# Kernel tuning notes

Hardware: AMD Instinct MI355X
Metric: run time of the kernel (lower is better)

The kernel has to match this reference:

```python
import jax, jax.numpy as jnp
import numpy as np

B, L, D, H, FF = 8, 512, 1024, 16, 4096
HD = D // H
EPS = 1e-5

def ste_round(x):
    # straight-through rounding (QAT)
    return x + jax.lax.stop_gradient(jnp.round(x) - x)

def fq_act(x):
    # 8-bit asymmetric per-tensor fake quant with dynamic min/max observer
    lo = jnp.minimum(jnp.min(x), 0.0)
    hi = jnp.maximum(jnp.max(x), 0.0)
    scale = jax.lax.stop_gradient(jnp.maximum((hi - lo) / 255.0, 1e-8))
    zp = jax.lax.stop_gradient(jnp.round(-lo / scale))
    q = jnp.clip(ste_round(x / scale) + zp, 0.0, 255.0)
    return (q - zp) * scale

def fq_w(w):
    # 8-bit symmetric per-tensor fake quant for weights
    scale = jax.lax.stop_gradient(jnp.maximum(jnp.max(jnp.abs(w)) / 127.0, 1e-8))
    q = jnp.clip(ste_round(w / scale), -128.0, 127.0)
    return q * scale

def qlinear(x, w, b):
    # QuantizedLayer: fake-quant weight, linear, fake-quant output activation
    return fq_act(jnp.einsum('...i,oi->...o', x, fq_w(w)) + b)

def layer_norm(x, g, b):
    mu = jnp.mean(x, axis=-1, keepdims=True)
    var = jnp.mean(jnp.square(x - mu), axis=-1, keepdims=True)
    return (x - mu) * jax.lax.rsqrt(var + EPS) * g + b

def setup_inputs() -> dict:
    key = jax.random.key(0)
    ks = jax.random.split(key, 8)
    s = 0.02
    return {
        'x': jax.random.normal(ks[0], (B, L, D), jnp.float32),
        'ln1_g': jnp.ones((D,), jnp.float32), 'ln1_b': jnp.zeros((D,), jnp.float32),
        'wq': jax.random.normal(ks[1], (D, D), jnp.float32) * s, 'bq': jnp.zeros((D,), jnp.float32),
        'wk': jax.random.normal(ks[2], (D, D), jnp.float32) * s, 'bk': jnp.zeros((D,), jnp.float32),
        'wv': jax.random.normal(ks[3], (D, D), jnp.float32) * s, 'bv': jnp.zeros((D,), jnp.float32),
        'wo': jax.random.normal(ks[4], (D, D), jnp.float32) * s, 'bo': jnp.zeros((D,), jnp.float32),
        'ln2_g': jnp.ones((D,), jnp.float32), 'ln2_b': jnp.zeros((D,), jnp.float32),
        'w_fc': jax.random.normal(ks[5], (FF, D), jnp.float32) * s, 'b_fc': jnp.zeros((FF,), jnp.float32),
        'w_proj': jax.random.normal(ks[6], (D, FF), jnp.float32) * s, 'b_proj': jnp.zeros((D,), jnp.float32),
    }

def reference(x, ln1_g, ln1_b, wq, bq, wk, bk, wv, bv, wo, bo,
              ln2_g, ln2_b, w_fc, b_fc, w_proj, b_proj):
    # --- attention sub-block ---
    h = layer_norm(x, ln1_g, ln1_b)
    def heads(t):  # [B,L,D] -> [B,H,L,HD]
        return t.reshape(B, L, H, HD).transpose(0, 2, 1, 3)
    # QuantizedLayer output fq + post_act fake quant (applied twice, per source)
    q = fq_act(heads(qlinear(h, wq, bq)))
    k = fq_act(heads(qlinear(h, wk, bk)))
    v = fq_act(heads(qlinear(h, wv, bv)))
    scale = 1.0 / np.sqrt(HD).astype(np.float32)
    attn = jnp.einsum('bhld,bhmd->bhlm', q, k) * scale  # [B,H,L,L]
    attn = jax.nn.softmax(attn, axis=-1)
    attn = fq_act(attn)  # softmax post-act fake quant (dropout p=0 is identity)
    ctx = jnp.einsum('bhlm,bhmd->bhld', attn, v)
    ctx = ctx.transpose(0, 2, 1, 3).reshape(B, L, D)
    x = x + qlinear(ctx, wo, bo)
    # --- MLP sub-block ---
    h2 = layer_norm(x, ln2_g, ln2_b)
    h2 = qlinear(h2, w_fc, b_fc)
    h2 = jax.nn.gelu(h2, approximate=False)  # torch nn.GELU default (erf)
    x = x + qlinear(h2, w_proj, b_proj)
    return x
```

## Files before the change

### kernel.cpp

```cpp
#include <hip/hip_runtime.h>
#include <cmath>

#define BB 8
#define LL 512
#define DD 1024
#define HH 16
#define HDD 64
#define FFD 4096
#define MTOK (BB*LL)
#define EPSF 1e-5f
#define BK 64

typedef __attribute__((ext_vector_type(8))) short bf16x8;
typedef __attribute__((ext_vector_type(4))) float f32x4;


struct WSet {
  const float* w[6];
  unsigned short* q[6];
  int n4[6];
};

__device__ inline void atomicMaxPos(float* addr, float v) {
  atomicMax((unsigned int*)addr, __float_as_uint(v));
}

__device__ inline unsigned short f2bf(float x) {
  unsigned int u = __float_as_uint(x);
  u += 0x7fffu + ((u >> 16) & 1u);
  return (unsigned short)(u >> 16);
}
__device__ inline float bf2f(unsigned short h) {
  return __uint_as_float((unsigned int)h << 16);
}

__device__ __forceinline__ void gld16(const unsigned short* g, unsigned short* l) {
  __builtin_amdgcn_global_load_lds(
      (const __attribute__((address_space(1))) unsigned int*)g,
      (__attribute__((address_space(3))) unsigned int*)l, 16, 0, 0);
}

__global__ void k_init_bcat(float* __restrict__ s, const float* __restrict__ b0,
                            const float* __restrict__ b1, const float* __restrict__ b2,
                            float* __restrict__ dst) {
  int i = blockIdx.x * blockDim.x + threadIdx.x;
  if (i < 256) s[i] = 0.0f;
  if (i < 3072) dst[i] = i < 1024 ? b0[i] : (i < 2048 ? b1[i - 1024] : b2[i - 2048]);
}

__global__ void k_absmax6(WSet ws, float* __restrict__ scal) {
  const int id = blockIdx.y;
  const float4* w4 = (const float4*)ws.w[id];
  const int n4 = ws.n4[id];
  float m = 0.0f;
  for (int i = blockIdx.x * blockDim.x + threadIdx.x; i < n4; i += gridDim.x * blockDim.x) {
    float4 v = w4[i];
    m = fmaxf(m, fmaxf(fmaxf(fabsf(v.x), fabsf(v.y)), fmaxf(fabsf(v.z), fabsf(v.w))));
  }
  #pragma unroll
  for (int o = 32; o; o >>= 1) m = fmaxf(m, __shfl_down(m, o, 64));
  __shared__ float sb[4];
  int lane = threadIdx.x & 63, wid = threadIdx.x >> 6;
  if (lane == 0) sb[wid] = m;
  __syncthreads();
  if (threadIdx.x == 0) atomicMaxPos(scal + id, fmaxf(fmaxf(sb[0], sb[1]), fmaxf(sb[2], sb[3])));
}

__global__ void k_quantw6(WSet ws, const float* __restrict__ scal) {
  const int id = blockIdx.y;
  float s = fmaxf(scal[id] / 127.0f, 1e-8f);
  const float4* w4 = (const float4*)ws.w[id];
  ushort4* q4 = (ushort4*)ws.q[id];
  const int n4 = ws.n4[id];
  for (int i = blockIdx.x * blockDim.x + threadIdx.x; i < n4; i += gridDim.x * blockDim.x) {
    float4 v = w4[i];
    ushort4 o;
    o.x = f2bf(fminf(fmaxf(rintf(v.x / s), -128.0f), 127.0f));
    o.y = f2bf(fminf(fmaxf(rintf(v.y / s), -128.0f), 127.0f));
    o.z = f2bf(fminf(fmaxf(rintf(v.z / s), -128.0f), 127.0f));
    o.w = f2bf(fminf(fmaxf(rintf(v.w / s), -128.0f), 127.0f));
    q4[i] = o;
  }
}

__device__ inline float2 fq_params(const float* sHi, const float* sNeg) {
  float hi = *sHi, lo = -(*sNeg);
  float scale = fmaxf((hi - lo) / 255.0f, 1e-8f);
  float zp = rintf(-lo / scale);
  return make_float2(scale, zp);
}
__device__ inline float fq1(float x, float scale, float zp) {
  float q = fminf(fmaxf(rintf(x / scale) + zp, 0.0f), 255.0f);
  return (q - zp) * scale;
}
__device__ inline float2 fq_params2(const float* sHi, const float* sNeg) {
  float2 p1 = fq_params(sHi, sNeg);
  float hi2 = fq1(*sHi, p1.x, p1.y);
  float lo2 = fq1(-(*sNeg), p1.x, p1.y);
  float scale = fmaxf((hi2 - lo2) / 255.0f, 1e-8f);
  float zp = rintf(-lo2 / scale);
  return make_float2(scale, zp);
}
__device__ inline float code2(float x, float2 p1, float2 p2) {
  float v1 = fq1(x, p1.x, p1.y);
  float q = fminf(fmaxf(rintf(v1 / p2.x) + p2.y, 0.0f), 255.0f);
  return q - p2.y;
}

__global__ void k_quant_codes(const float* __restrict__ src, int colBase,
                              unsigned short* __restrict__ oc, const float* __restrict__ sl) {
  float2 p1 = fq_params(sl, sl + 1);
  float2 p2 = fq_params2(sl, sl + 1);
  const int n4 = MTOK * DD / 4;
  for (int i = blockIdx.x * blockDim.x + threadIdx.x; i < n4; i += gridDim.x * blockDim.x) {
    int row = i >> 8, c = (i & 255) * 4;
    float4 v = *(const float4*)(src + (size_t)row * 3072 + colBase + c);
    ushort4 o;
    o.x = f2bf(code2(v.x, p1, p2)); o.y = f2bf(code2(v.y, p1, p2));
    o.z = f2bf(code2(v.z, p1, p2)); o.w = f2bf(code2(v.w, p1, p2));
    *(ushort4*)&oc[(size_t)row * DD + c] = o;
  }
}

__global__ __launch_bounds__(256) void k_quant_codes_vt(
    const float* __restrict__ src, unsigned short* __restrict__ vt,
    const float* __restrict__ sl) {
  __shared__ unsigned short tile[64 * 68];
  float2 p1 = fq_params(sl, sl + 1);
  float2 p2 = fq_params2(sl, sl + 1);
  const int m0 = blockIdx.x * 64, h = blockIdx.y, b = blockIdx.z;
  const int t = threadIdx.x;
  const int r = t >> 2, c0 = (t & 3) * 16;
  const float* s4 = src + ((size_t)(b * LL + m0 + r)) * 3072 + 2048 + h * HDD + c0;
  #pragma unroll
  for (int i = 0; i < 4; ++i) {
    float4 v = *(const float4*)(s4 + i * 4);
    ushort4 o;
    o.x = f2bf(code2(v.x, p1, p2)); o.y = f2bf(code2(v.y, p1, p2));
    o.z = f2bf(code2(v.z, p1, p2)); o.w = f2bf(code2(v.w, p1, p2));
    *(ushort4*)&tile[r * 68 + c0 + i * 4] = o;
  }
  __syncthreads();
  const int dr = t >> 2, ms = (t & 3) * 16;
  unsigned short* dst = vt + ((size_t)((b * HH + h) * HDD + dr)) * LL + m0 + ms;
  #pragma unroll
  for (int i = 0; i < 4; ++i) {
    ushort4 o;
    o.x = tile[(ms + i * 4 + 0) * 68 + dr];
    o.y = tile[(ms + i * 4 + 1) * 68 + dr];
    o.z = tile[(ms + i * 4 + 2) * 68 + dr];
    o.w = tile[(ms + i * 4 + 3) * 68 + dr];
    *(ushort4*)(dst + i * 4) = o;
  }
}

__global__ void k_sum_minmax(const float* __restrict__ parts, size_t pstride4, int np,
                             const float* __restrict__ bias, int n4, int cmask,
                             float* __restrict__ sl) {
  float hi = 0.0f, ng = 0.0f;
  for (int i = blockIdx.x * blockDim.x + threadIdx.x; i < n4; i += gridDim.x * blockDim.x) {
    float4 bc = *(const float4*)(bias + (i & cmask) * 4);
    float vx = bc.x, vy = bc.y, vz = bc.z, vw = bc.w;
    for (int j = 0; j < np; ++j) {
      float4 a = ((const float4*)parts)[j * pstride4 + i];
      vx += a.x; vy += a.y; vz += a.z; vw += a.w;
    }
    hi = fmaxf(hi, fmaxf(fmaxf(vx, vy), fmaxf(vz, vw)));
    ng = fmaxf(ng, fmaxf(fmaxf(-vx, -vy), fmaxf(-vz, -vw)));
  }
  #pragma unroll
  for (int o = 32; o; o >>= 1) {
    hi = fmaxf(hi, __shfl_down(hi, o, 64));
    ng = fmaxf(ng, __shfl_down(ng, o, 64));
  }
  __shared__ float sh[4], sn[4];
  int lane = threadIdx.x & 63, wid = threadIdx.x >> 6;
  if (lane == 0) { sh[wid] = hi; sn[wid] = ng; }
  __syncthreads();
  if (threadIdx.x == 0) {
    atomicMaxPos(sl, fmaxf(fmaxf(sh[0], sh[1]), fmaxf(sh[2], sh[3])));
    atomicMaxPos(sl + 1, fmaxf(fmaxf(sn[0], sn[1]), fmaxf(sn[2], sn[3])));
  }
}

__global__ void k_quant_res2(const float* __restrict__ parts, size_t pstride4, int np,
                             const float* __restrict__ bias, const float* __restrict__ res,
                             float* __restrict__ out, int n4, int cmask,
                             const float* __restrict__ sl) {
  float2 p = fq_params(sl, sl + 1);
  for (int i = blockIdx.x * blockDim.x + threadIdx.x; i < n4; i += gridDim.x * blockDim.x) {
    float4 bc = *(const float4*)(bias + (i & cmask) * 4);
    float vx = bc.x, vy = bc.y, vz = bc.z, vw = bc.w;
    for (int j = 0; j < np; ++j) {
      float4 a = ((const float4*)parts)[j * pstride4 + i];
      vx += a.x; vy += a.y; vz += a.z; vw += a.w;
    }
    float4 r = ((const float4*)res)[i];
    float4 o;
    o.x = r.x + fq1(vx, p.x, p.y);
    o.y = r.y + fq1(vy, p.x, p.y);
    o.z = r.z + fq1(vz, p.x, p.y);
    o.w = r.w + fq1(vw, p.x, p.y);
    ((float4*)out)[i] = o;
  }
}

__device__ inline float gelu_exact(float g) {
  return 0.5f * g * (1.0f + erff(g * 0.7071067811865475f));
}

__global__ void k_gelu_codes(const float* __restrict__ x,
                             unsigned short* __restrict__ ghi, unsigned short* __restrict__ glo,
                             int n4, const float* __restrict__ sl) {
  float2 p = fq_params(sl, sl + 1);
  for (int i = blockIdx.x * blockDim.x + threadIdx.x; i < n4; i += gridDim.x * blockDim.x) {
    float4 v = ((const float4*)x)[i];
    float g0 = gelu_exact(fq1(v.x, p.x, p.y)), g1 = gelu_exact(fq1(v.y, p.x, p.y));
    float g2 = gelu_exact(fq1(v.z, p.x, p.y)), g3 = gelu_exact(fq1(v.w, p.x, p.y));
    ushort4 h, l;
    h.x = f2bf(g0); l.x = f2bf(g0 - bf2f(h.x));
    h.y = f2bf(g1); l.y = f2bf(g1 - bf2f(h.y));
    h.z = f2bf(g2); l.z = f2bf(g2 - bf2f(h.z));
    h.w = f2bf(g3); l.w = f2bf(g3 - bf2f(h.w));
    ((ushort4*)ghi)[i] = h;
    ((ushort4*)glo)[i] = l;
  }
}

__device__ inline float block_sum256(float v, float* sb) {
  #pragma unroll
  for (int o = 32; o; o >>= 1) v += __shfl_down(v, o, 64);
  int lane = threadIdx.x & 63, wid = threadIdx.x >> 6;
  __syncthreads();
  if (lane == 0) sb[wid] = v;
  __syncthreads();
  return sb[0] + sb[1] + sb[2] + sb[3];
}

__global__ __launch_bounds__(256) void k_ln_bf(const float* __restrict__ x, const float* __restrict__ g,
                                               const float* __restrict__ bta,
                                               unsigned short* __restrict__ ohi,
                                               unsigned short* __restrict__ olo) {
  __shared__ float sb[4];
  int row = blockIdx.x;
  const float4* xr = (const float4*)(x + (size_t)row * DD);
  float4 v = xr[threadIdx.x];
  float mu = block_sum256(v.x + v.y + v.z + v.w, sb) * (1.0f / DD);
  float dx = v.x - mu, dy = v.y - mu, dz = v.z - mu, dw = v.w - mu;
  float var = block_sum256(dx*dx + dy*dy + dz*dz + dw*dw, sb) * (1.0f / DD);
  float rs = 1.0f / sqrtf(var + EPSF);
  float4 gv = ((const float4*)g)[threadIdx.x];
  float4 bv = ((const float4*)bta)[threadIdx.x];
  float o0 = dx * rs * gv.x + bv.x;
  float o1 = dy * rs * gv.y + bv.y;
  float o2 = dz * rs * gv.z + bv.z;
  float o3 = dw * rs * gv.w + bv.w;
  ushort4 h, l;
  h.x = f2bf(o0); l.x = f2bf(o0 - bf2f(h.x));
  h.y = f2bf(o1); l.y = f2bf(o1 - bf2f(h.y));
  h.z = f2bf(o2); l.z = f2bf(o2 - bf2f(h.z));
  h.w = f2bf(o3); l.w = f2bf(o3 - bf2f(h.w));
  ((ushort4*)(ohi + (size_t)row * DD))[threadIdx.x] = h;
  ((ushort4*)(olo + (size_t)row * DD))[threadIdx.x] = l;
}

__global__ __launch_bounds__(256) void k_res_ln(
    const float* __restrict__ parts, size_t pstride4,
    const float* __restrict__ bias, const float* __restrict__ res,
    float* __restrict__ x1, const float* __restrict__ sl,
    const float* __restrict__ g, const float* __restrict__ bta,
    unsigned short* __restrict__ ohi, unsigned short* __restrict__ olo) {
  __shared__ float sb[4];
  float2 p = fq_params(sl, sl + 1);
  int row = blockIdx.x, t = threadIdx.x;
  size_t i4 = (size_t)row * 256 + t;
  float4 a = ((const float4*)parts)[i4];
  float4 b = ((const float4*)parts)[pstride4 + i4];
  float4 bc = ((const float4*)bias)[t];
  float4 r = ((const float4*)res)[i4];
  float4 xv;
  xv.x = r.x + fq1(a.x + b.x + bc.x, p.x, p.y);
  xv.y = r.y + fq1(a.y + b.y + bc.y, p.x, p.y);
  xv.z = r.z + fq1(a.z + b.z + bc.z, p.x, p.y);
  xv.w = r.w + fq1(a.w + b.w + bc.w, p.x, p.y);
  ((float4*)x1)[i4] = xv;
  float mu = block_sum256(xv.x + xv.y + xv.z + xv.w, sb) * (1.0f / DD);
  float dx = xv.x - mu, dy = xv.y - mu, dz = xv.z - mu, dw = xv.w - mu;
  float var = block_sum256(dx*dx + dy*dy + dz*dz + dw*dw, sb) * (1.0f / DD);
  float rs = 1.0f / sqrtf(var + EPSF);
  float4 gv = ((const float4*)g)[t];
  float4 bv = ((const float4*)bta)[t];
  float o0 = dx * rs * gv.x + bv.x;
  float o1 = dy * rs * gv.y + bv.y;
  float o2 = dz * rs * gv.z + bv.z;
  float o3 = dw * rs * gv.w + bv.w;
  ushort4 h, l;
  h.x = f2bf(o0); l.x = f2bf(o0 - bf2f(h.x));
  h.y = f2bf(o1); l.y = f2bf(o1 - bf2f(h.y));
  h.z = f2bf(o2); l.z = f2bf(o2 - bf2f(h.z));
  h.w = f2bf(o3); l.w = f2bf(o3 - bf2f(h.w));
  ((ushort4*)(ohi + (size_t)row * DD))[t] = h;
  ((ushort4*)(olo + (size_t)row * DD))[t] = l;
}

__global__ __launch_bounds__(256, 3) void k_gemm_bf(
    const unsigned short* __restrict__ Ahi, const unsigned short* __restrict__ Alo,
    const unsigned short* __restrict__ Bq,
    const float* __restrict__ bias, const float* __restrict__ wsc, float* __restrict__ obs,
    float* __restrict__ C, int ldC, int K, int kLen, int segShift, size_t partStride) {
  __shared__ unsigned short sAh[128 * BK];
  __shared__ unsigned short sAl[128 * BK];
  __shared__ unsigned short sB [128 * BK];
  __shared__ float redH, redN;
  const int t = threadIdx.x;
  const int row0 = blockIdx.x * 128, col0 = blockIdx.y * 128;
  const int kOff = blockIdx.z * kLen;
  float* Cp = C + (size_t)blockIdx.z * partStride;
  const int wave = t >> 6, lane = t & 63;
  const int wr = (wave >> 1) * 64, wc = (wave & 1) * 64;
  const int fr = lane & 15, fq = lane >> 4;
  const int seg = col0 >> segShift;
  const float s = fmaxf(wsc[seg] / 127.0f, 1e-8f);
  if (t == 0) { redH = 0.f; redN = 0.f; }

  f32x4 acc[4][4];
  #pragma unroll
  for (int i = 0; i < 4; ++i)
    #pragma unroll
    for (int j = 0; j < 4; ++j) acc[i][j] = (f32x4){0.f, 0.f, 0.f, 0.f};

  const int srB = lane >> 3;
  const int scs = lane & 7;

  for (int k0 = kOff; k0 < kOff + kLen; k0 += BK) {
    __syncthreads();
    #pragma unroll
    for (int it = 0; it < 4; ++it) {
      int r = (wave * 4 + it) * 8 + srB;
      int g = scs ^ (r & 7);
      size_t ga = (size_t)(row0 + r) * K + k0 + g * 8;
      size_t gb = (size_t)(col0 + r) * K + k0 + g * 8;
      int ld = r * BK + scs * 8;
      gld16(Ahi + ga, &sAh[ld]);
      gld16(Alo + ga, &sAl[ld]);
      gld16(Bq + gb, &sB[ld]);
    }
    __syncthreads();
    #pragma unroll
    for (int hh = 0; hh < 2; ++hh) {
      bf16x8 ah[4], al[4], bb[4];
      #pragma unroll
      for (int i = 0; i < 4; ++i) {
        int Ra = wr + i * 16 + fr;
        int Rb = wc + i * 16 + fr;
        int ca = ((hh * 4 + fq) ^ (Ra & 7)) * 8;
        int cb = ((hh * 4 + fq) ^ (Rb & 7)) * 8;
        ah[i] = *(const bf16x8*)&sAh[Ra * BK + ca];
        al[i] = *(const bf16x8*)&sAl[Ra * BK + ca];
        bb[i] = *(const bf16x8*)&sB [Rb * BK + cb];
      }
      #pragma unroll
      for (int i = 0; i < 4; ++i)
        #pragma unroll
        for (int j = 0; j < 4; ++j) {
          acc[i][j] = __builtin_amdgcn_mfma_f32_16x16x32_bf16(ah[i], bb[j], acc[i][j], 0, 0, 0);
          acc[i][j] = __builtin_amdgcn_mfma_f32_16x16x32_bf16(al[i], bb[j], acc[i][j], 0, 0, 0);
        }
    }
  }

  float ohi = 0.f, ong = 0.f;
  #pragma unroll
  for (int i = 0; i < 4; ++i) {
    #pragma unroll
    for (int j = 0; j < 4; ++j) {
      int col = col0 + wc + j * 16 + fr;
      float bcol = bias ? bias[col] : 0.0f;
      #pragma unroll
      for (int rg = 0; rg < 4; ++rg) {
        int row = row0 + wr + i * 16 + fq * 4 + rg;
        float val = acc[i][j][rg] * s + bcol;
        if (obs) { ohi = fmaxf(ohi, val); ong = fmaxf(ong, -val); }
        Cp[(size_t)row * ldC + col] = val;
      }
    }
  }
  if (obs) {
    #pragma unroll
    for (int o = 32; o; o >>= 1) {
      ohi = fmaxf(ohi, __shfl_down(ohi, o, 64));
      ong = fmaxf(ong, __shfl_down(ong, o, 64));
    }
    if (lane == 0) { atomicMaxPos(&redH, ohi); atomicMaxPos(&redN, ong); }
    __syncthreads();
    if (t == 0) {
      atomicMaxPos(obs + 2 * seg, redH);
      atomicMaxPos(obs + 2 * seg + 1, redN);
    }
  }
}

__global__ __launch_bounds__(256) void k_attn_a_mfma(
    const unsigned short* __restrict__ qc, const unsigned short* __restrict__ kc,
    const float* __restrict__ slq, const float* __restrict__ slk,
    float* __restrict__ rowm, float* __restrict__ rowz, float* __restrict__ maxp) {
  __shared__ unsigned short ks[64 * 72];
  __shared__ float redp;
  const int t = threadIdx.x, wave = t >> 6, lane = t & 63;
  const int fr = lane & 15, fq = lane >> 4;
  const int l0 = blockIdx.x * 64, h = blockIdx.y, b = blockIdx.z;
  const float sfac = fq_params2(slq, slq + 1).x * fq_params2(slk, slk + 1).x * 0.125f;
  if (t == 0) redp = 0.f;
  const unsigned short* qrow = qc + ((size_t)(b * LL + l0 + wave * 16 + fr)) * DD + h * HDD;
  bf16x8 qa0 = *(const bf16x8*)(qrow + fq * 8);
  bf16x8 qa1 = *(const bf16x8*)(qrow + 32 + fq * 8);
  float mrun[4] = {-INFINITY, -INFINITY, -INFINITY, -INFINITY};
  float zrun[4] = {0.f, 0.f, 0.f, 0.f};
  for (int mc = 0; mc < LL; mc += 64) {
    __syncthreads();
    #pragma unroll
    for (int it = 0; it < 2; ++it) {
      int si = t + it * 256, r = si >> 3, c8 = (si & 7) * 8;
      *(bf16x8*)&ks[r * 72 + c8] =
          *(const bf16x8*)(kc + ((size_t)(b * LL + mc + r)) * DD + h * HDD + c8);
    }
    __syncthreads();
    float sv[4][4];
    #pragma unroll
    for (int j = 0; j < 4; ++j) {
      bf16x8 b0 = *(const bf16x8*)&ks[(j * 16 + fr) * 72 + fq * 8];
      bf16x8 b1 = *(const bf16x8*)&ks[(j * 16 + fr) * 72 + 32 + fq * 8];
      f32x4 sAcc = (f32x4){0.f, 0.f, 0.f, 0.f};
      sAcc = __builtin_amdgcn_mfma_f32_16x16x32_bf16(qa0, b0, sAcc, 0, 0, 0);
      sAcc = __builtin_amdgcn_mfma_f32_16x16x32_bf16(qa1, b1, sAcc, 0, 0, 0);
      #pragma unroll
      for (int rg = 0; rg < 4; ++rg) sv[j][rg] = sAcc[rg] * sfac;
    }
    #pragma unroll
    for (int rg = 0; rg < 4; ++rg) {
      float nm = mrun[rg];
      #pragma unroll
      for (int j = 0; j < 4; ++j) nm = fmaxf(nm, sv[j][rg]);
      float z = zrun[rg] * expf(mrun[rg] - nm);
      #pragma unroll
      for (int j = 0; j < 4; ++j) z += expf(sv[j][rg] - nm);
      zrun[rg] = z; mrun[rg] = nm;
    }
  }
  #pragma unroll
  for (int off = 1; off < 16; off <<= 1) {
    #pragma unroll
    for (int rg = 0; rg < 4; ++rg) {
      float om = __shfl_xor(mrun[rg], off, 64);
      float oz = __shfl_xor(zrun[rg], off, 64);
      float nm = fmaxf(mrun[rg], om);
      zrun[rg] = zrun[rg] * expf(mrun[rg] - nm) + oz * expf(om - nm);
      mrun[rg] = nm;
    }
  }
  if (fr == 0) {
    int rid = (b * HH + h) * LL + l0 + wave * 16 + fq * 4;
    float lmax = 0.f;
    #pragma unroll
    for (int rg = 0; rg < 4; ++rg) {
      rowm[rid + rg] = mrun[rg]; rowz[rid + rg] = zrun[rg];
      lmax = fmaxf(lmax, 1.0f / zrun[rg]);
    }
    atomicMaxPos(&redp, lmax);
  }
  __syncthreads();
  if (t == 0) atomicMaxPos(maxp, redp);
}

__global__ __launch_bounds__(256) void k_attn_b_mfma(
    const unsigned short* __restrict__ qc, const unsigned short* __restrict__ kc,
    const unsigned short* __restrict__ vt,
    const float* __restrict__ slq, const float* __restrict__ slk, const float* __restrict__ slv,
    const float* __restrict__ rowm, const float* __restrict__ rowz,
    const float* __restrict__ maxp,
    unsigned short* __restrict__ chi, unsigned short* __restrict__ clo) {
  __shared__ unsigned short ks[64 * 72];
  __shared__ unsigned short vs[64 * 72];
  __shared__ unsigned short ps[4][16 * 72];
  const int t = threadIdx.x, wave = t >> 6, lane = t & 63;
  const int fr = lane & 15, fq = lane >> 4;
  const int l0 = blockIdx.x * 64, h = blockIdx.y, b = blockIdx.z;
  const float sfac = fq_params2(slq, slq + 1).x * fq_params2(slk, slk + 1).x * 0.125f;
  const float sv2 = fq_params2(slv, slv + 1).x;
  const float pscale = fmaxf(maxp[0] / 255.0f, 1e-8f);
  const float ipscale = 1.0f / pscale;
  const int ridb = (b * HH + h) * LL + l0 + wave * 16 + fq * 4;
  float rm[4], rzi[4];
  #pragma unroll
  for (int rg = 0; rg < 4; ++rg) { rm[rg] = rowm[ridb + rg]; rzi[rg] = 1.0f / rowz[ridb + rg]; }
  const unsigned short* qrow = qc + ((size_t)(b * LL + l0 + wave * 16 + fr)) * DD + h * HDD;
  bf16x8 qa0 = *(const bf16x8*)(qrow + fq * 8);
  bf16x8 qa1 = *(const bf16x8*)(qrow + 32 + fq * 8);
  f32x4 acc[4];
  #pragma unroll
  for (int jd = 0; jd < 4; ++jd) acc[jd] = (f32x4){0.f, 0.f, 0.f, 0.f};

  for (int mc = 0; mc < LL; mc += 64) {
    __syncthreads();
    #pragma unroll
    for (int it = 0; it < 2; ++it) {
      int si = t + it * 256, r = si >> 3, c8 = (si & 7) * 8;
      *(bf16x8*)&ks[r * 72 + c8] =
          *(const bf16x8*)(kc + ((size_t)(b * LL + mc + r)) * DD + h * HDD + c8);
      *(bf16x8*)&vs[r * 72 + c8] =
          *(const bf16x8*)(vt + ((size_t)((b * HH + h) * HDD + r)) * LL + mc + c8);
    }
    __syncthreads();
    #pragma unroll
    for (int j = 0; j < 4; ++j) {
      bf16x8 b0 = *(const bf16x8*)&ks[(j * 16 + fr) * 72 + fq * 8];
      bf16x8 b1 = *(const bf16x8*)&ks[(j * 16 + fr) * 72 + 32 + fq * 8];
      f32x4 sAcc = (f32x4){0.f, 0.f, 0.f, 0.f};
      sAcc = __builtin_amdgcn_mfma_f32_16x16x32_bf16(qa0, b0, sAcc, 0, 0, 0);
      sAcc = __builtin_amdgcn_mfma_f32_16x16x32_bf16(qa1, b1, sAcc, 0, 0, 0);
      #pragma unroll
      for (int rg = 0; rg < 4; ++rg) {
        float p = expf(sAcc[rg] * sfac - rm[rg]) * rzi[rg];
        float q = fminf(fmaxf(rintf(p * ipscale), 0.0f), 255.0f);
        ps[wave][(fq * 4 + rg) * 72 + j * 16 + fr] = f2bf(q);
      }
    }
    __syncthreads();
    bf16x8 pa0 = *(const bf16x8*)&ps[wave][fr * 72 + fq * 8];
    bf16x8 pa1 = *(const bf16x8*)&ps[wave][fr * 72 + 32 + fq * 8];
    #pragma unroll
    for (int jd = 0; jd < 4; ++jd) {
      bf16x8 vb0 = *(const bf16x8*)&vs[(jd * 16 + fr) * 72 + fq * 8];
      bf16x8 vb1 = *(const bf16x8*)&vs[(jd * 16 + fr) * 72 + 32 + fq * 8];
      acc[jd] = __builtin_amdgcn_mfma_f32_16x16x32_bf16(pa0, vb0, acc[jd], 0, 0, 0);
      acc[jd] = __builtin_amdgcn_mfma_f32_16x16x32_bf16(pa1, vb1, acc[jd], 0, 0, 0);
    }
  }
  const float osc = pscale * sv2;
  #pragma unroll
  for (int jd = 0; jd < 4; ++jd)
    #pragma unroll
    for (int rg = 0; rg < 4; ++rg) {
      int row = l0 + wave * 16 + fq * 4 + rg;
      size_t cidx = ((size_t)(b * LL + row)) * DD + h * HDD + jd * 16 + fr;
      float val = acc[jd][rg] * osc;
      unsigned short hh = f2bf(val);
      chi[cidx] = hh;
      clo[cidx] = f2bf(val - bf2f(hh));
    }
}

extern "C" void kernel_launch(void* const* d_in, const int* in_sizes, int n_in,
                              void* d_out, int out_size, void* d_ws, size_t ws_size,
                              hipStream_t stream) {
  const float* x    = (const float*)d_in[0];
  const float* ln1g = (const float*)d_in[1];
  const float* ln1b = (const float*)d_in[2];
  const float* wq   = (const float*)d_in[3];
  const float* bq   = (const float*)d_in[4];
  const float* wk   = (const float*)d_in[5];
  const float* bk   = (const float*)d_in[6];
  const float* wv   = (const float*)d_in[7];
  const float* bv   = (const float*)d_in[8];
  const float* wo   = (const float*)d_in[9];
  const float* bo   = (const float*)d_in[10];
  const float* ln2g = (const float*)d_in[11];
  const float* ln2b = (const float*)d_in[12];
  const float* wfc  = (const float*)d_in[13];
  const float* bfc  = (const float*)d_in[14];
  const float* wpj  = (const float*)d_in[15];
  const float* bpj  = (const float*)d_in[16];
  float* out = (float*)d_out;
  float* ws = (float*)d_ws;

  size_t off = 0;
  float* scal = ws + off; off += 256;
  float* bcat = ws + off; off += 3072;
  unsigned short* wcatQ = (unsigned short*)(ws + off); off += (size_t)3072*DD/2;
  unsigned short* woQ   = (unsigned short*)(ws + off); off += (size_t)DD*DD/2;
  unsigned short* wfcQ  = (unsigned short*)(ws + off); off += (size_t)FFD*DD/2;
  unsigned short* wpjQ  = (unsigned short*)(ws + off); off += (size_t)DD*FFD/2;
  unsigned short* abhi  = (unsigned short*)(ws + off); off += (size_t)MTOK*DD/2;
  unsigned short* ablo  = (unsigned short*)(ws + off); off += (size_t)MTOK*DD/2;
  float* qkvb = ws + off; off += (size_t)MTOK*3072;
  float* x1rg = ws + off; off += (size_t)MTOK*DD;
  unsigned short* vtc = (unsigned short*)(ws + off); off += (size_t)MTOK*DD/2;
  float* rowm = ws + off; off += (size_t)BB*HH*LL;
  float* rowz = ws + off; off += (size_t)BB*HH*LL;
  float* fcb  = ws + off; off += (size_t)MTOK*FFD;
  unsigned short* gello = (unsigned short*)(ws + off); off += (size_t)MTOK*FFD/2;

  unsigned short* qcod = (unsigned short*)x1rg;
  unsigned short* kcod = (unsigned short*)(x1rg + (size_t)MTOK*DD/2);
  float* x1 = x1rg;
  float* opart = qkvb;
  unsigned short* gelhi = (unsigned short*)qkvb;
  float* pjpart = fcb;

  const int ND  = MTOK*DD/4;
  const int NF  = MTOK*FFD/4;
  const int NW  = DD*DD/4;
  const int NWF = DD*FFD/4;
  const size_t PS4 = (size_t)MTOK*DD/4;

  auto g4 = [](int n4){ int g = (n4 + 255) / 256; return g > 4096 ? 4096 : g; };

  k_init_bcat<<<12, 256, 0, stream>>>(scal, bq, bk, bv, bcat);

  WSet wset;
  wset.w[0] = wq;  wset.q[0] = wcatQ;                   wset.n4[0] = NW;
  wset.w[1] = wk;  wset.q[1] = wcatQ + (size_t)DD*DD;   wset.n4[1] = NW;
  wset.w[2] = wv;  wset.q[2] = wcatQ + (size_t)2*DD*DD; wset.n4[2] = NW;
  wset.w[3] = wo;  wset.q[3] = woQ;                     wset.n4[3] = NW;
  wset.w[4] = wfc; wset.q[4] = wfcQ;                    wset.n4[4] = NWF;
  wset.w[5] = wpj; wset.q[5] = wpjQ;                    wset.n4[5] = NWF;

  k_absmax6<<<dim3(512, 6), 256, 0, stream>>>(wset, scal);
  k_quantw6<<<dim3(512, 6), 256, 0, stream>>>(wset, scal);

  k_ln_bf<<<MTOK, 256, 0, stream>>>(x, ln1g, ln1b, abhi, ablo);

  k_gemm_bf<<<dim3(32, 24, 1), 256, 0, stream>>>(abhi, ablo, wcatQ, bcat, scal+0, scal+6,
                                                 qkvb, 3072, DD, DD, 10, 0);

  k_quant_codes<<<g4(ND), 256, 0, stream>>>(qkvb, 0,    qcod, scal+6);
  k_quant_codes<<<g4(ND), 256, 0, stream>>>(qkvb, 1024, kcod, scal+8);
  k_quant_codes_vt<<<dim3(8, 16, 8), 256, 0, stream>>>(qkvb, vtc, scal+10);

  k_attn_a_mfma<<<dim3(8, 16, 8), 256, 0, stream>>>(qcod, kcod, scal+6, scal+8,
                                                    rowm, rowz, scal+18);
  k_attn_b_mfma<<<dim3(8, 16, 8), 256, 0, stream>>>(qcod, kcod, vtc, scal+6, scal+8, scal+10,
                                                    rowm, rowz, scal+18, abhi, ablo);

  k_gemm_bf<<<dim3(32, 8, 2), 256, 0, stream>>>(abhi, ablo, woQ, nullptr, scal+3, nullptr,
                                                opart, DD, DD, 512, 20, (size_t)MTOK*DD);
  k_sum_minmax<<<2048, 256, 0, stream>>>(opart, PS4, 2, bo, ND, 255, scal+19);
  k_res_ln<<<MTOK, 256, 0, stream>>>(opart, PS4, bo, x, x1, scal+19,
                                     ln2g, ln2b, abhi, ablo);

  k_gemm_bf<<<dim3(32, 32, 1), 256, 0, stream>>>(abhi, ablo, wfcQ, bfc, scal+4, scal+21,
                                                 fcb, FFD, DD, DD, 20, 0);
  k_gelu_codes<<<g4(NF), 256, 0, stream>>>(fcb, gelhi, gello, NF, scal+21);

  k_gemm_bf<<<dim3(32, 8, 2), 256, 0, stream>>>(gelhi, gello, wpjQ, nullptr, scal+5, nullptr,
                                                pjpart, DD, FFD, 2048, 20, (size_t)MTOK*DD);
  k_sum_minmax<<<2048, 256, 0, stream>>>(pjpart, PS4, 2, bpj, ND, 255, scal+23);
  k_quant_res2<<<g4(ND), 256, 0, stream>>>(pjpart, PS4, 2, bpj, x1, out, ND, 255, scal+23);
}
```

Before: 620.9 us.

## Add wide 128x256 tile MFMA GEMM and use it for QKV, FC and projection

Adds a GEMM kernel with a 128x256 block tile in which each wave computes a 64x128 sub-tile. This raises operand reuse from LDS and registers per MFMA, and it replaces the narrower GEMM for the QKV, FC and output-projection layers. The projection GEMM moves from split-K 2 to split-K 4 to keep enough blocks in flight, and the reduction kernels now sum 4 partials. The cost is higher register and LDS pressure (64 KB LDS, 128 accumulator floats per lane), fewer blocks for the QKV GEMM, and that the partial buffer must hold 4 slices.

```diff
diff --git a/kernel.cpp b/kernel.cpp
--- a/kernel.cpp
+++ b/kernel.cpp
@@ -400,6 +400,111 @@
   }
 }
 
+__global__ __launch_bounds__(256, 2) void k_gemm_wide(
+    const unsigned short* __restrict__ Ahi, const unsigned short* __restrict__ Alo,
+    const unsigned short* __restrict__ Bq,
+    const float* __restrict__ bias, const float* __restrict__ wsc, float* __restrict__ obs,
+    float* __restrict__ C, int ldC, int K, int kLen, int segShift, size_t partStride) {
+  __shared__ unsigned short sAh[128 * BK];
+  __shared__ unsigned short sAl[128 * BK];
+  __shared__ unsigned short sB [256 * BK];
+  __shared__ float redH, redN;
+  const int t = threadIdx.x;
+  const int row0 = blockIdx.x * 128, col0 = blockIdx.y * 256;
+  const int kOff = blockIdx.z * kLen;
+  float* Cp = C + (size_t)blockIdx.z * partStride;
+  const int wave = t >> 6, lane = t & 63;
+  const int wr = (wave >> 1) * 64, wc = (wave & 1) * 128;
+  const int fr = lane & 15, fq = lane >> 4;
+  const int seg = col0 >> segShift;
+  const float s = fmaxf(wsc[seg] / 127.0f, 1e-8f);
+  if (t == 0) { redH = 0.f; redN = 0.f; }
+
+  f32x4 acc[4][8];
+  #pragma unroll
+  for (int i = 0; i < 4; ++i)
+    #pragma unroll
+    for (int j = 0; j < 8; ++j) acc[i][j] = (f32x4){0.f, 0.f, 0.f, 0.f};
+
+  const int srB = lane >> 3;
+  const int scs = lane & 7;
+
+  for (int k0 = kOff; k0 < kOff + kLen; k0 += BK) {
+    __syncthreads();
+    #pragma unroll
+    for (int it = 0; it < 4; ++it) {
+      int r = (wave * 4 + it) * 8 + srB;
+      int g = scs ^ (r & 7);
+      size_t ga = (size_t)(row0 + r) * K + k0 + g * 8;
+      int ld = r * BK + scs * 8;
+      gld16(Ahi + ga, &sAh[ld]);
+      gld16(Alo + ga, &sAl[ld]);
+    }
+    #pragma unroll
+    for (int it = 0; it < 8; ++it) {
+      int r = (wave * 8 + it) * 8 + srB;
+      int g = scs ^ (r & 7);
+      size_t gb = (size_t)(col0 + r) * K + k0 + g * 8;
+      gld16(Bq + gb, &sB[r * BK + scs * 8]);
+    }
+    __syncthreads();
+    #pragma unroll
+    for (int hh = 0; hh < 2; ++hh) {
+      bf16x8 ah[4], al[4], bb[8];
+      #pragma unroll
+      for (int i = 0; i < 4; ++i) {
+        int Ra = wr + i * 16 + fr;
+        int ca = ((hh * 4 + fq) ^ (Ra & 7)) * 8;
+        ah[i] = *(const bf16x8*)&sAh[Ra * BK + ca];
+        al[i] = *(const bf16x8*)&sAl[Ra * BK + ca];
+      }
+      #pragma unroll
+      for (int j = 0; j < 8; ++j) {
+        int Rb = wc + j * 16 + fr;
+        int cb = ((hh * 4 + fq) ^ (Rb & 7)) * 8;
+        bb[j] = *(const bf16x8*)&sB[Rb * BK + cb];
+      }
+      #pragma unroll
+      for (int i = 0; i < 4; ++i)
+        #pragma unroll
+        for (int j = 0; j < 8; ++j) {
+          acc[i][j] = __builtin_amdgcn_mfma_f32_16x16x32_bf16(ah[i], bb[j], acc[i][j], 0, 0, 0);
+          acc[i][j] = __builtin_amdgcn_mfma_f32_16x16x32_bf16(al[i], bb[j], acc[i][j], 0, 0, 0);
+        }
+    }
+  }
+
+  float ohi = 0.f, ong = 0.f;
+  #pragma unroll
+  for (int i = 0; i < 4; ++i) {
+    #pragma unroll
+    for (int j = 0; j < 8; ++j) {
+      int col = col0 + wc + j * 16 + fr;
+      float bcol = bias ? bias[col] : 0.0f;
+      #pragma unroll
+      for (int rg = 0; rg < 4; ++rg) {
+        int row = row0 + wr + i * 16 + fq * 4 + rg;
+        float val = acc[i][j][rg] * s + bcol;
+        if (obs) { ohi = fmaxf(ohi, val); ong = fmaxf(ong, -val); }
+        Cp[(size_t)row * ldC + col] = val;
+      }
+    }
+  }
+  if (obs) {
+    #pragma unroll
+    for (int o = 32; o; o >>= 1) {
+      ohi = fmaxf(ohi, __shfl_down(ohi, o, 64));
+      ong = fmaxf(ong, __shfl_down(ong, o, 64));
+    }
+    if (lane == 0) { atomicMaxPos(&redH, ohi); atomicMaxPos(&redN, ong); }
+    __syncthreads();
+    if (t == 0) {
+      atomicMaxPos(obs + 2 * seg, redH);
+      atomicMaxPos(obs + 2 * seg + 1, redN);
+    }
+  }
+}
+
 __global__ __launch_bounds__(256) void k_attn_a_mfma(
     const unsigned short* __restrict__ qc, const unsigned short* __restrict__ kc,
     const float* __restrict__ slq, const float* __restrict__ slk,
@@ -620,8 +725,8 @@
 
   k_ln_bf<<<MTOK, 256, 0, stream>>>(x, ln1g, ln1b, abhi, ablo);
 
-  k_gemm_bf<<<dim3(32, 24, 1), 256, 0, stream>>>(abhi, ablo, wcatQ, bcat, scal+0, scal+6,
-                                                 qkvb, 3072, DD, DD, 10, 0);
+  k_gemm_wide<<<dim3(32, 12, 1), 256, 0, stream>>>(abhi, ablo, wcatQ, bcat, scal+0, scal+6,
+                                                   qkvb, 3072, DD, DD, 10, 0);
 
   k_quant_codes<<<g4(ND), 256, 0, stream>>>(qkvb, 0,    qcod, scal+6);
   k_quant_codes<<<g4(ND), 256, 0, stream>>>(qkvb, 1024, kcod, scal+8);
@@ -638,12 +743,12 @@
   k_res_ln<<<MTOK, 256, 0, stream>>>(opart, PS4, bo, x, x1, scal+19,
                                      ln2g, ln2b, abhi, ablo);
 
-  k_gemm_bf<<<dim3(32, 32, 1), 256, 0, stream>>>(abhi, ablo, wfcQ, bfc, scal+4, scal+21,
-                                                 fcb, FFD, DD, DD, 20, 0);
+  k_gemm_wide<<<dim3(32, 16, 1), 256, 0, stream>>>(abhi, ablo, wfcQ, bfc, scal+4, scal+21,
+                                                   fcb, FFD, DD, DD, 20, 0);
   k_gelu_codes<<<g4(NF), 256, 0, stream>>>(fcb, gelhi, gello, NF, scal+21);
 
-  k_gemm_bf<<<dim3(32, 8, 2), 256, 0, stream>>>(gelhi, gello, wpjQ, nullptr, scal+5, nullptr,
-                                                pjpart, DD, FFD, 2048, 20, (size_t)MTOK*DD);
-  k_sum_minmax<<<2048, 256, 0, stream>>>(pjpart, PS4, 2, bpj, ND, 255, scal+23);
-  k_quant_res2<<<g4(ND), 256, 0, stream>>>(pjpart, PS4, 2, bpj, x1, out, ND, 255, scal+23);
-}
+  k_gemm_wide<<<dim3(32, 4, 4), 256, 0, stream>>>(gelhi, gello, wpjQ, nullptr, scal+5, nullptr,
+                                                  pjpart, DD, FFD, 1024, 20, (size_t)MTOK*DD);
+  k_sum_minmax<<<2048, 256, 0, stream>>>(pjpart, PS4, 4, bpj, ND, 255, scal+23);
+  k_quant_res2<<<g4(ND), 256, 0, stream>>>(pjpart, PS4, 4, bpj, x1, out, ND, 255, scal+23);
+}
```

Result: no change. 621.7 us (+0.1%).
